# Kernel optimization log

Measured on AMD Instinct MI355X. Metric: run time of the kernel, lower is better.

## Reference

```python
import jax, jax.numpy as jnp
import numpy as np

B, H, S, D = 4, 8, 2048, 64  # batch, heads, seq, head_dim (feature_dim == num_features == D)


def setup_inputs() -> dict:
    key = jax.random.key(0)
    kq, kk, kv, kw = jax.random.split(key, 4)
    return {
        "q": jax.random.normal(kq, (B, H, S, D), dtype=jnp.float32),
        "k": jax.random.normal(kk, (B, H, S, D), dtype=jnp.float32),
        "v": jax.random.normal(kv, (B, H, S, D), dtype=jnp.float32),
        "random_weights": jax.random.normal(kw, (D, D), dtype=jnp.float32),  # [feature_dim, num_features]
    }


def reference(q, k, v, random_weights):
    # F.linear(x, W) == x @ W.T ; W: [feature_dim, num_features]
    qf = jax.nn.relu(jnp.einsum('bnhd,fd->bnhf', q, random_weights))
    kf = jax.nn.relu(jnp.einsum('bnad,fd->bnaf', k, random_weights))
    # full [B, N, S_q, S_kv] score matrix (as the original materializes it)
    scores = jnp.einsum('bnhd,bnad->bnha', qf, kf)
    attn_weights = jax.nn.softmax(scores, axis=-1)
    # NOTE: faithful to the original (buggy) einsum: m is contracted only in attn,
    # so attn_output[b,n,h,d] = v[b,n,h,d] * sum_m attn[b,n,h,m]
    attn_output = jnp.einsum('bnhm,bnhd->bnhd', attn_weights, v)
    return (attn_output, attn_weights)
```

## Files before the change

### kernel.cpp

```cpp
#include <hip/hip_runtime.h>
#include <cstddef>
#include <cstdint>

#define SEQ   2048
#define DIM   64
#define NHEAD 32
#define BM    128
#define BN    128
#define NT    (SEQ / BN)
#define WLD   68

typedef __attribute__((ext_vector_type(8))) short short8v;
typedef __attribute__((ext_vector_type(4))) float f32x4;

__device__ __forceinline__ unsigned short f2bf(float x) {
    union { float f; unsigned u; } v; v.f = x;
    unsigned r = v.u + 0x7FFFu + ((v.u >> 16) & 1u);
    return (unsigned short)(r >> 16);
}
__device__ __forceinline__ float bf2f(unsigned short h) {
    union { unsigned u; float f; } v; v.u = ((unsigned)h) << 16;
    return v.f;
}

__device__ __forceinline__ void gl_lds16(const void* g, void* l) {
    __builtin_amdgcn_global_load_lds(
        (const __attribute__((address_space(1))) unsigned int*)g,
        (__attribute__((address_space(3))) unsigned int*)l,
        16, 0, 0);
}

__global__ __launch_bounds__(256) void kfsplit_kernel(const float* __restrict__ kin,
                                                      const float* __restrict__ W,
                                                      unsigned short* __restrict__ khg,
                                                      unsigned short* __restrict__ klg)
{
    __shared__ __align__(16) float Ws[64 * WLD];
    const int tid  = threadIdx.x;
    const int head = blockIdx.x >> 4;
    const int r0   = (blockIdx.x & 15) * BM;

    {
        const int f = tid >> 2, cc = (tid & 3) * 16;
        const float* gw = W + f * DIM + cc;
        #pragma unroll
        for (int kk = 0; kk < 4; ++kk)
            *reinterpret_cast<float4*>(&Ws[f * WLD + cc + kk * 4]) =
                *reinterpret_cast<const float4*>(gw + kk * 4);
    }
    __syncthreads();

    const int lane = tid & 63;
    const int wid  = tid >> 6;
    const float* kb = kin + ((size_t)head * SEQ + r0) * DIM;

    float acc0[16], acc1[16];
    #pragma unroll
    for (int j = 0; j < 16; ++j) { acc0[j] = 0.f; acc1[j] = 0.f; }

    for (int d4 = 0; d4 < 16; ++d4) {
        const float4 x0 = *reinterpret_cast<const float4*>(kb + (size_t)lane * DIM + d4 * 4);
        const float4 x1 = *reinterpret_cast<const float4*>(kb + (size_t)(64 + lane) * DIM + d4 * 4);
        #pragma unroll
        for (int j = 0; j < 16; ++j) {
            const float4 w4 = *reinterpret_cast<const float4*>(&Ws[(wid * 16 + j) * WLD + d4 * 4]);
            acc0[j] = fmaf(x0.x, w4.x, fmaf(x0.y, w4.y, fmaf(x0.z, w4.z, fmaf(x0.w, w4.w, acc0[j]))));
            acc1[j] = fmaf(x1.x, w4.x, fmaf(x1.y, w4.y, fmaf(x1.z, w4.z, fmaf(x1.w, w4.w, acc1[j]))));
        }
    }

#define SPLIT_ROW(ACC, ROWOFF)                                                          \
    do {                                                                                \
        unsigned hp[8], lp[8];                                                          \
        _Pragma("unroll")                                                               \
        for (int j2 = 0; j2 < 8; ++j2) {                                                \
            const float kf0 = fmaxf(ACC[2 * j2], 0.f);                                  \
            const float kf1 = fmaxf(ACC[2 * j2 + 1], 0.f);                              \
            const unsigned short h0 = f2bf(kf0), h1 = f2bf(kf1);                        \
            const unsigned short l0 = f2bf(kf0 - bf2f(h0));                             \
            const unsigned short l1 = f2bf(kf1 - bf2f(h1));                             \
            hp[j2] = (unsigned)h0 | ((unsigned)h1 << 16);                               \
            lp[j2] = (unsigned)l0 | ((unsigned)l1 << 16);                               \
        }                                                                               \
        unsigned short* dh = khg + ((size_t)head * SEQ + r0 + (ROWOFF)) * DIM + wid * 16; \
        unsigned short* dl = klg + ((size_t)head * SEQ + r0 + (ROWOFF)) * DIM + wid * 16; \
        uint4 a, b;                                                                     \
        a.x = hp[0]; a.y = hp[1]; a.z = hp[2]; a.w = hp[3];                             \
        b.x = hp[4]; b.y = hp[5]; b.z = hp[6]; b.w = hp[7];                             \
        *reinterpret_cast<uint4*>(dh) = a; *reinterpret_cast<uint4*>(dh + 8) = b;       \
        a.x = lp[0]; a.y = lp[1]; a.z = lp[2]; a.w = lp[3];                             \
        b.x = lp[4]; b.y = lp[5]; b.z = lp[6]; b.w = lp[7];                             \
        *reinterpret_cast<uint4*>(dl) = a; *reinterpret_cast<uint4*>(dl + 8) = b;       \
    } while (0)

    SPLIT_ROW(acc0, lane);
    SPLIT_ROW(acc1, 64 + lane);
#undef SPLIT_ROW
}

__global__ __launch_bounds__(256, 2) void attn_kernel(const float* __restrict__ q,
                                                      const float* __restrict__ W,
                                                      const unsigned short* __restrict__ khg,
                                                      const unsigned short* __restrict__ klg,
                                                      float* __restrict__ out)
{
    __shared__ __align__(16) unsigned char lds_raw[67584];
    float* Ws   = (float*)lds_raw;
    float* qf   = (float*)(lds_raw + 32768);
    float* mbuf = (float*)(lds_raw + 65536);
    float* lbuf = (float*)(lds_raw + 66560);

    const int tid  = threadIdx.x;
    const int head = blockIdx.x >> 4;
    const int r0   = (blockIdx.x & 15) * BM;
    const int lane = tid & 63;
    const int wid  = tid >> 6;

    const size_t khead_b = (size_t)head * SEQ * DIM * 2;
    const unsigned char* gkh = (const unsigned char*)khg + khead_b;
    const unsigned char* gkl = (const unsigned char*)klg + khead_b;

#define STAGE(BUF, T)                                                                   \
    do {                                                                                \
        const unsigned char* skh = gkh + (size_t)(T) * (BN * DIM * 2);                  \
        const unsigned char* skl = gkl + (size_t)(T) * (BN * DIM * 2);                  \
        unsigned char* lkh = lds_raw + (BUF) * 32768;                                   \
        unsigned char* lkl = lkh + 16384;                                               \
        _Pragma("unroll")                                                               \
        for (int i_ = 0; i_ < 4; ++i_) {                                                \
            const unsigned o_   = wid * 4096 + i_ * 1024 + lane * 16;                   \
            const unsigned row_ = o_ >> 7;                                              \
            const unsigned u_   = (o_ & ~127u) | ((o_ & 127u) ^ ((row_ & 7u) << 4));    \
            gl_lds16(skh + u_, lkh + wid * 4096 + i_ * 1024);                           \
            gl_lds16(skl + u_, lkl + wid * 4096 + i_ * 1024);                           \
        }                                                                               \
    } while (0)

    {
        const int f = tid >> 2, cc = (tid & 3) * 16;
        const float* gw = W + f * DIM + cc;
        #pragma unroll
        for (int kk = 0; kk < 4; ++kk)
            *reinterpret_cast<float4*>(&Ws[f * WLD + cc + kk * 4]) =
                *reinterpret_cast<const float4*>(gw + kk * 4);
    }
    __syncthreads();

    {
        const float* qb = q + ((size_t)head * SEQ + r0) * DIM;
        float a0[16], a1[16];
        #pragma unroll
        for (int j = 0; j < 16; ++j) { a0[j] = 0.f; a1[j] = 0.f; }
        for (int d4 = 0; d4 < 16; ++d4) {
            const float4 x0 = *reinterpret_cast<const float4*>(qb + (size_t)lane * DIM + d4 * 4);
            const float4 x1 = *reinterpret_cast<const float4*>(qb + (size_t)(64 + lane) * DIM + d4 * 4);
            #pragma unroll
            for (int j = 0; j < 16; ++j) {
                const float4 w4 = *reinterpret_cast<const float4*>(&Ws[(wid * 16 + j) * WLD + d4 * 4]);
                a0[j] = fmaf(x0.x, w4.x, fmaf(x0.y, w4.y, fmaf(x0.z, w4.z, fmaf(x0.w, w4.w, a0[j]))));
                a1[j] = fmaf(x1.x, w4.x, fmaf(x1.y, w4.y, fmaf(x1.z, w4.z, fmaf(x1.w, w4.w, a1[j]))));
            }
        }
        #pragma unroll
        for (int j = 0; j < 16; ++j) {
            qf[(size_t)lane * WLD + wid * 16 + j]        = fmaxf(a0[j], 0.f);
            qf[(size_t)(64 + lane) * WLD + wid * 16 + j] = fmaxf(a1[j], 0.f);
        }
    }
    __syncthreads();

    STAGE(0, 0);

    const int lr = lane & 15, lh = lane >> 4;
    const int wrow = (wid >> 1) * 64, wcol = (wid & 1) * 64;
    short8v qh[4][2], ql[4][2];
    #pragma unroll
    for (int rf = 0; rf < 4; ++rf)
        #pragma unroll
        for (int ks = 0; ks < 2; ++ks) {
            const float* src = &qf[(size_t)(wrow + rf * 16 + lr) * WLD + ks * 32 + lh * 8];
            short8v h, l;
            #pragma unroll
            for (int e = 0; e < 8; ++e) {
                const float x = src[e];
                const unsigned short hh = f2bf(x);
                h[e] = (short)hh;
                l[e] = (short)f2bf(x - bf2f(hh));
            }
            qh[rf][ks] = h;
            ql[rf][ks] = l;
        }
    __syncthreads();

#define COMPUTE_ACC(BUF)                                                                  \
    do {                                                                                  \
        const unsigned char* khb = lds_raw + (BUF) * 32768;                               \
        const unsigned char* klb = khb + 16384;                                           \
        _Pragma("unroll")                                                                 \
        for (int cf = 0; cf < 4; ++cf) {                                                  \
            const int c  = wcol + cf * 16 + lr;                                           \
            const int rb = c * 128 + lh * 16;                                             \
            const int sw = (c & 7) << 4;                                                  \
            const short8v bh0 = *reinterpret_cast<const short8v*>(khb + ((rb) ^ sw));     \
            const short8v bh1 = *reinterpret_cast<const short8v*>(khb + ((rb + 64) ^ sw));\
            const short8v bl0 = *reinterpret_cast<const short8v*>(klb + ((rb) ^ sw));     \
            const short8v bl1 = *reinterpret_cast<const short8v*>(klb + ((rb + 64) ^ sw));\
            _Pragma("unroll")                                                             \
            for (int rf = 0; rf < 4; ++rf) {                                              \
                f32x4 a = acc[rf][cf];                                                    \
                a = __builtin_amdgcn_mfma_f32_16x16x32_bf16(qh[rf][0], bh0, a, 0, 0, 0);  \
                a = __builtin_amdgcn_mfma_f32_16x16x32_bf16(ql[rf][0], bh0, a, 0, 0, 0);  \
                a = __builtin_amdgcn_mfma_f32_16x16x32_bf16(qh[rf][0], bl0, a, 0, 0, 0);  \
                a = __builtin_amdgcn_mfma_f32_16x16x32_bf16(qh[rf][1], bh1, a, 0, 0, 0);  \
                a = __builtin_amdgcn_mfma_f32_16x16x32_bf16(ql[rf][1], bh1, a, 0, 0, 0);  \
                a = __builtin_amdgcn_mfma_f32_16x16x32_bf16(qh[rf][1], bl1, a, 0, 0, 0);  \
                acc[rf][cf] = a;                                                          \
            }                                                                             \
        }                                                                                 \
    } while (0)

    float mrow[16], lrow[16];
    #pragma unroll
    for (int i = 0; i < 16; ++i) { mrow[i] = -INFINITY; lrow[i] = 0.f; }

    {
        int cur = 0;
        for (int t = 0; t < NT; ++t) {
            if (t + 1 < NT) STAGE(cur ^ 1, t + 1);
            f32x4 acc[4][4] = {};
            COMPUTE_ACC(cur);
            #pragma unroll
            for (int rf = 0; rf < 4; ++rf)
                #pragma unroll
                for (int q4 = 0; q4 < 4; ++q4) {
                    const int i = rf * 4 + q4;
                    const float v0 = acc[rf][0][q4], v1 = acc[rf][1][q4];
                    const float v2 = acc[rf][2][q4], v3 = acc[rf][3][q4];
                    const float tm = fmaxf(fmaxf(v0, v1), fmaxf(v2, v3));
                    const float mn = fmaxf(mrow[i], tm);
                    const float p = __expf(v0 - mn) + __expf(v1 - mn) +
                                    __expf(v2 - mn) + __expf(v3 - mn);
                    lrow[i] = lrow[i] * __expf(mrow[i] - mn) + p;
                    mrow[i] = mn;
                }
            __syncthreads();
            cur ^= 1;
        }
    }

    STAGE(0, 0);

    #pragma unroll
    for (int s = 0; s < 4; ++s) {
        const int msk = 1 << s;
        #pragma unroll
        for (int i = 0; i < 16; ++i) {
            const float m2 = __shfl_xor(mrow[i], msk);
            const float l2 = __shfl_xor(lrow[i], msk);
            const float mn = fmaxf(mrow[i], m2);
            lrow[i] = lrow[i] * __expf(mrow[i] - mn) + l2 * __expf(m2 - mn);
            mrow[i] = mn;
        }
    }

    if (lr == 0) {
        #pragma unroll
        for (int i = 0; i < 16; ++i) {
            const int row16 = (i >> 2) * 16 + lh * 4 + (i & 3);
            mbuf[wid * 64 + row16] = mrow[i];
            lbuf[wid * 64 + row16] = lrow[i];
        }
    }
    __syncthreads();
    {
        const int pw = wid ^ 1;
        #pragma unroll
        for (int i = 0; i < 16; ++i) {
            const int row16 = (i >> 2) * 16 + lh * 4 + (i & 3);
            const float m2 = mbuf[pw * 64 + row16];
            const float l2 = lbuf[pw * 64 + row16];
            const float mn = fmaxf(mrow[i], m2);
            lrow[i] = lrow[i] * __expf(mrow[i] - mn) + l2 * __expf(m2 - mn);
            mrow[i] = mn;
        }
    }
    #pragma unroll
    for (int i = 0; i < 16; ++i) lrow[i] = 1.0f / lrow[i];

    float* outp = out + ((size_t)head * SEQ + r0) * SEQ;
    {
        int cur = 0;
        for (int t = 0; t < NT; ++t) {
            if (t + 1 < NT) STAGE(cur ^ 1, t + 1);
            f32x4 acc[4][4] = {};
            COMPUTE_ACC(cur);
            const int col0 = t * BN + wcol;
            #pragma unroll
            for (int rf = 0; rf < 4; ++rf)
                #pragma unroll
                for (int q4 = 0; q4 < 4; ++q4) {
                    const int i = rf * 4 + q4;
                    const int row = wrow + rf * 16 + lh * 4 + q4;
                    float* rp = outp + (size_t)row * SEQ + col0 + lr;
                    rp[0]  = __expf(acc[rf][0][q4] - mrow[i]) * lrow[i];
                    rp[16] = __expf(acc[rf][1][q4] - mrow[i]) * lrow[i];
                    rp[32] = __expf(acc[rf][2][q4] - mrow[i]) * lrow[i];
                    rp[48] = __expf(acc[rf][3][q4] - mrow[i]) * lrow[i];
                }
            __syncthreads();
            cur ^= 1;
        }
    }
#undef STAGE
#undef COMPUTE_ACC
}

extern "C" void kernel_launch(void* const* d_in, const int* in_sizes, int n_in,
                              void* d_out, int out_size, void* d_ws, size_t ws_size,
                              hipStream_t stream)
{
    const float* q = (const float*)d_in[0];
    const float* k = (const float*)d_in[1];
    const float* v = (const float*)d_in[2];
    const float* W = (const float*)d_in[3];
    float* out = (float*)d_out;

    const size_t nkf = (size_t)NHEAD * SEQ * DIM;
    unsigned short* kh;
    if (d_ws != nullptr && ws_size >= nkf * 4u) {
        kh = (unsigned short*)d_ws;
    } else {
        kh = (unsigned short*)out;
    }
    unsigned short* kl = kh + nkf;
    float* attn = out + nkf;

    kfsplit_kernel<<<NHEAD * (SEQ / BM), 256, 0, stream>>>(k, W, kh, kl);
    attn_kernel<<<NHEAD * (SEQ / BM), 256, 0, stream>>>(q, W, kh, kl, attn);

    hipMemcpyAsync((void*)out, (const void*)v, nkf * sizeof(float),
                   hipMemcpyDeviceToDevice, stream);
}
```

Before: 653.3 us.

## Transpose MFMA operands so each lane owns a row; use exp2 and float4 stores

Swaps the A/B operands of the score MFMAs so the accumulator holds Kᵀ·Q. Each lane then holds four consecutive columns of a single query row, which allows vectorized float4 stores of the large attention-weight output and shrinks per-lane softmax state from 16 rows to 4. The LOG2E scale is folded into the Q features so native exp2 replaces __expf, and the cross-lane reductions change to shuffles at distances 16 and 32. Scaling Q by log2e before the bf16 hi/lo split slightly changes rounding.

```diff
diff --git a/kernel.cpp b/kernel.cpp
--- a/kernel.cpp
+++ b/kernel.cpp
@@ -9,9 +9,12 @@
 #define BN    128
 #define NT    (SEQ / BN)
 #define WLD   68
+#define LOG2E 1.44269504088896340736f
 
 typedef __attribute__((ext_vector_type(8))) short short8v;
 typedef __attribute__((ext_vector_type(4))) float f32x4;
+
+__device__ __forceinline__ float fexp2(float x) { return __builtin_amdgcn_exp2f(x); }
 
 __device__ __forceinline__ unsigned short f2bf(float x) {
     union { float f; unsigned u; } v; v.f = x;
@@ -163,8 +166,8 @@
         }
         #pragma unroll
         for (int j = 0; j < 16; ++j) {
-            qf[(size_t)lane * WLD + wid * 16 + j]        = fmaxf(a0[j], 0.f);
-            qf[(size_t)(64 + lane) * WLD + wid * 16 + j] = fmaxf(a1[j], 0.f);
+            qf[(size_t)lane * WLD + wid * 16 + j]        = fmaxf(a0[j] * LOG2E, 0.f);
+            qf[(size_t)(64 + lane) * WLD + wid * 16 + j] = fmaxf(a1[j] * LOG2E, 0.f);
         }
     }
     __syncthreads();
@@ -175,10 +178,10 @@
     const int wrow = (wid >> 1) * 64, wcol = (wid & 1) * 64;
     short8v qh[4][2], ql[4][2];
     #pragma unroll
-    for (int rf = 0; rf < 4; ++rf)
+    for (int cf = 0; cf < 4; ++cf)
         #pragma unroll
         for (int ks = 0; ks < 2; ++ks) {
-            const float* src = &qf[(size_t)(wrow + rf * 16 + lr) * WLD + ks * 32 + lh * 8];
+            const float* src = &qf[(size_t)(wrow + cf * 16 + lr) * WLD + ks * 32 + lh * 8];
             short8v h, l;
             #pragma unroll
             for (int e = 0; e < 8; ++e) {
@@ -187,8 +190,8 @@
                 h[e] = (short)hh;
                 l[e] = (short)f2bf(x - bf2f(hh));
             }
-            qh[rf][ks] = h;
-            ql[rf][ks] = l;
+            qh[cf][ks] = h;
+            ql[cf][ks] = l;
         }
     __syncthreads();
 
@@ -197,31 +200,31 @@
         const unsigned char* khb = lds_raw + (BUF) * 32768;                               \
         const unsigned char* klb = khb + 16384;                                           \
         _Pragma("unroll")                                                                 \
-        for (int cf = 0; cf < 4; ++cf) {                                                  \
-            const int c  = wcol + cf * 16 + lr;                                           \
+        for (int rf = 0; rf < 4; ++rf) {                                                  \
+            const int c  = wcol + rf * 16 + lr;                                           \
             const int rb = c * 128 + lh * 16;                                             \
             const int sw = (c & 7) << 4;                                                  \
-            const short8v bh0 = *reinterpret_cast<const short8v*>(khb + ((rb) ^ sw));     \
-            const short8v bh1 = *reinterpret_cast<const short8v*>(khb + ((rb + 64) ^ sw));\
-            const short8v bl0 = *reinterpret_cast<const short8v*>(klb + ((rb) ^ sw));     \
-            const short8v bl1 = *reinterpret_cast<const short8v*>(klb + ((rb + 64) ^ sw));\
+            const short8v ah0 = *reinterpret_cast<const short8v*>(khb + ((rb) ^ sw));     \
+            const short8v ah1 = *reinterpret_cast<const short8v*>(khb + ((rb + 64) ^ sw));\
+            const short8v al0 = *reinterpret_cast<const short8v*>(klb + ((rb) ^ sw));     \
+            const short8v al1 = *reinterpret_cast<const short8v*>(klb + ((rb + 64) ^ sw));\
             _Pragma("unroll")                                                             \
-            for (int rf = 0; rf < 4; ++rf) {                                              \
+            for (int cf = 0; cf < 4; ++cf) {                                              \
                 f32x4 a = acc[rf][cf];                                                    \
-                a = __builtin_amdgcn_mfma_f32_16x16x32_bf16(qh[rf][0], bh0, a, 0, 0, 0);  \
-                a = __builtin_amdgcn_mfma_f32_16x16x32_bf16(ql[rf][0], bh0, a, 0, 0, 0);  \
-                a = __builtin_amdgcn_mfma_f32_16x16x32_bf16(qh[rf][0], bl0, a, 0, 0, 0);  \
-                a = __builtin_amdgcn_mfma_f32_16x16x32_bf16(qh[rf][1], bh1, a, 0, 0, 0);  \
-                a = __builtin_amdgcn_mfma_f32_16x16x32_bf16(ql[rf][1], bh1, a, 0, 0, 0);  \
-                a = __builtin_amdgcn_mfma_f32_16x16x32_bf16(qh[rf][1], bl1, a, 0, 0, 0);  \
+                a = __builtin_amdgcn_mfma_f32_16x16x32_bf16(ah0, qh[cf][0], a, 0, 0, 0);  \
+                a = __builtin_amdgcn_mfma_f32_16x16x32_bf16(ah0, ql[cf][0], a, 0, 0, 0);  \
+                a = __builtin_amdgcn_mfma_f32_16x16x32_bf16(al0, qh[cf][0], a, 0, 0, 0);  \
+                a = __builtin_amdgcn_mfma_f32_16x16x32_bf16(ah1, qh[cf][1], a, 0, 0, 0);  \
+                a = __builtin_amdgcn_mfma_f32_16x16x32_bf16(ah1, ql[cf][1], a, 0, 0, 0);  \
+                a = __builtin_amdgcn_mfma_f32_16x16x32_bf16(al1, qh[cf][1], a, 0, 0, 0);  \
                 acc[rf][cf] = a;                                                          \
             }                                                                             \
         }                                                                                 \
     } while (0)
 
-    float mrow[16], lrow[16];
-    #pragma unroll
-    for (int i = 0; i < 16; ++i) { mrow[i] = -INFINITY; lrow[i] = 0.f; }
+    float m4[4], l4[4];
+    #pragma unroll
+    for (int i = 0; i < 4; ++i) { m4[i] = -INFINITY; l4[i] = 0.f; }
 
     {
         int cur = 0;
@@ -230,19 +233,25 @@
             f32x4 acc[4][4] = {};
             COMPUTE_ACC(cur);
             #pragma unroll
-            for (int rf = 0; rf < 4; ++rf)
+            for (int cf = 0; cf < 4; ++cf) {
+                float tm = fmaxf(fmaxf(acc[0][cf][0], acc[0][cf][1]),
+                                 fmaxf(acc[0][cf][2], acc[0][cf][3]));
                 #pragma unroll
-                for (int q4 = 0; q4 < 4; ++q4) {
-                    const int i = rf * 4 + q4;
-                    const float v0 = acc[rf][0][q4], v1 = acc[rf][1][q4];
-                    const float v2 = acc[rf][2][q4], v3 = acc[rf][3][q4];
-                    const float tm = fmaxf(fmaxf(v0, v1), fmaxf(v2, v3));
-                    const float mn = fmaxf(mrow[i], tm);
-                    const float p = __expf(v0 - mn) + __expf(v1 - mn) +
-                                    __expf(v2 - mn) + __expf(v3 - mn);
-                    lrow[i] = lrow[i] * __expf(mrow[i] - mn) + p;
-                    mrow[i] = mn;
+                for (int rf = 1; rf < 4; ++rf)
+                    tm = fmaxf(tm, fmaxf(fmaxf(acc[rf][cf][0], acc[rf][cf][1]),
+                                         fmaxf(acc[rf][cf][2], acc[rf][cf][3])));
+                const float mn = fmaxf(m4[cf], tm);
+                float p = 0.f;
+                #pragma unroll
+                for (int rf = 0; rf < 4; ++rf) {
+                    p += fexp2(acc[rf][cf][0] - mn);
+                    p += fexp2(acc[rf][cf][1] - mn);
+                    p += fexp2(acc[rf][cf][2] - mn);
+                    p += fexp2(acc[rf][cf][3] - mn);
                 }
+                l4[cf] = l4[cf] * fexp2(m4[cf] - mn) + p;
+                m4[cf] = mn;
+            }
             __syncthreads();
             cur ^= 1;
         }
@@ -251,41 +260,38 @@
     STAGE(0, 0);
 
     #pragma unroll
-    for (int s = 0; s < 4; ++s) {
-        const int msk = 1 << s;
-        #pragma unroll
-        for (int i = 0; i < 16; ++i) {
-            const float m2 = __shfl_xor(mrow[i], msk);
-            const float l2 = __shfl_xor(lrow[i], msk);
-            const float mn = fmaxf(mrow[i], m2);
-            lrow[i] = lrow[i] * __expf(mrow[i] - mn) + l2 * __expf(m2 - mn);
-            mrow[i] = mn;
-        }
-    }
-
-    if (lr == 0) {
-        #pragma unroll
-        for (int i = 0; i < 16; ++i) {
-            const int row16 = (i >> 2) * 16 + lh * 4 + (i & 3);
-            mbuf[wid * 64 + row16] = mrow[i];
-            lbuf[wid * 64 + row16] = lrow[i];
+    for (int s = 16; s <= 32; s <<= 1) {
+        #pragma unroll
+        for (int i = 0; i < 4; ++i) {
+            const float m2 = __shfl_xor(m4[i], s);
+            const float l2 = __shfl_xor(l4[i], s);
+            const float mn = fmaxf(m4[i], m2);
+            l4[i] = l4[i] * fexp2(m4[i] - mn) + l2 * fexp2(m2 - mn);
+            m4[i] = mn;
+        }
+    }
+
+    if (lh == 0) {
+        #pragma unroll
+        for (int i = 0; i < 4; ++i) {
+            mbuf[wid * 64 + i * 16 + lr] = m4[i];
+            lbuf[wid * 64 + i * 16 + lr] = l4[i];
         }
     }
     __syncthreads();
     {
         const int pw = wid ^ 1;
         #pragma unroll
-        for (int i = 0; i < 16; ++i) {
-            const int row16 = (i >> 2) * 16 + lh * 4 + (i & 3);
-            const float m2 = mbuf[pw * 64 + row16];
-            const float l2 = lbuf[pw * 64 + row16];
-            const float mn = fmaxf(mrow[i], m2);
-            lrow[i] = lrow[i] * __expf(mrow[i] - mn) + l2 * __expf(m2 - mn);
-            mrow[i] = mn;
-        }
-    }
-    #pragma unroll
-    for (int i = 0; i < 16; ++i) lrow[i] = 1.0f / lrow[i];
+        for (int i = 0; i < 4; ++i) {
+            const float m2 = mbuf[pw * 64 + i * 16 + lr];
+            const float l2 = lbuf[pw * 64 + i * 16 + lr];
+            const float mn = fmaxf(m4[i], m2);
+            l4[i] = l4[i] * fexp2(m4[i] - mn) + l2 * fexp2(m2 - mn);
+            m4[i] = mn;
+        }
+    }
+    #pragma unroll
+    for (int i = 0; i < 4; ++i) l4[i] = 1.0f / l4[i];
 
     float* outp = out + ((size_t)head * SEQ + r0) * SEQ;
     {
@@ -294,19 +300,21 @@
             if (t + 1 < NT) STAGE(cur ^ 1, t + 1);
             f32x4 acc[4][4] = {};
             COMPUTE_ACC(cur);
-            const int col0 = t * BN + wcol;
+            const int col0 = t * BN + wcol + lh * 4;
             #pragma unroll
-            for (int rf = 0; rf < 4; ++rf)
+            for (int cf = 0; cf < 4; ++cf) {
+                const float m = m4[cf], ri = l4[cf];
+                float* rowp = outp + (size_t)(wrow + cf * 16 + lr) * SEQ + col0;
                 #pragma unroll
-                for (int q4 = 0; q4 < 4; ++q4) {
-                    const int i = rf * 4 + q4;
-                    const int row = wrow + rf * 16 + lh * 4 + q4;
-                    float* rp = outp + (size_t)row * SEQ + col0 + lr;
-                    rp[0]  = __expf(acc[rf][0][q4] - mrow[i]) * lrow[i];
-                    rp[16] = __expf(acc[rf][1][q4] - mrow[i]) * lrow[i];
-                    rp[32] = __expf(acc[rf][2][q4] - mrow[i]) * lrow[i];
-                    rp[48] = __expf(acc[rf][3][q4] - mrow[i]) * lrow[i];
+                for (int rf = 0; rf < 4; ++rf) {
+                    float4 o;
+                    o.x = fexp2(acc[rf][cf][0] - m) * ri;
+                    o.y = fexp2(acc[rf][cf][1] - m) * ri;
+                    o.z = fexp2(acc[rf][cf][2] - m) * ri;
+                    o.w = fexp2(acc[rf][cf][3] - m) * ri;
+                    *reinterpret_cast<float4*>(rowp + rf * 16) = o;
                 }
+            }
             __syncthreads();
             cur ^= 1;
         }
```

Result: no change. 662.0 us (+1.3%).
